# Performance work log

Measured on AMD Instinct MI355X. Metric: run time of the kernel, lower is better.

The kernel has to match this reference:

```python
import jax, jax.numpy as jnp
import numpy as np

N_HEAD = 4
N_FEAT = 256
D_K = N_FEAT // N_HEAD


def setup_inputs() -> dict:
    key = jax.random.key(0)
    ks = jax.random.split(key, 7)
    B, T, F = 8, 2048, N_FEAT
    return {
        "query": jax.random.normal(ks[0], (B, T, F), dtype=jnp.float32),
        "key": jax.random.normal(ks[1], (B, T, F), dtype=jnp.float32),
        "value": jax.random.normal(ks[2], (B, T, F), dtype=jnp.float32),
        "mask": jax.random.randint(ks[3], (B, 1, T), 0, 2, dtype=jnp.int32),
        "W_qkv": jax.random.normal(ks[4], (3 * F, 3 * F), dtype=jnp.float32) * 0.02,
        "b_qkv": jnp.zeros((3 * F,), dtype=jnp.float32),
        "W_out": jax.random.normal(ks[5], (F, F), dtype=jnp.float32) * 0.02,
        "b_out": jnp.zeros((F,), dtype=jnp.float32),
    }


def reference(query, key, value, mask, W_qkv, b_qkv, W_out, b_out):
    B, T, F = query.shape
    H, dk = N_HEAD, D_K
    # fused QKV projection on concatenated [q; k; v]  -> (B, T, 3F)
    qkv = jnp.concatenate([query, key, value], axis=-1) @ W_qkv.T + b_qkv
    qkv = qkv.reshape(B, T, H, 3 * dk)
    q, k, v = jnp.split(qkv, 3, axis=-1)          # each (B, T, H, dk)
    q = q.transpose(0, 2, 1, 3)                    # (B, H, T, dk)
    k = k.transpose(0, 2, 1, 3)
    v = v.transpose(0, 2, 1, 3)
    scores = jnp.einsum("bhqd,bhkd->bhqk", q, k) / jnp.sqrt(jnp.float32(dk))
    # mask: (B, 1, T) -> broadcast (B, 1, 1, T); positions where mask==0 are masked
    m = (mask[:, None, :, :] == 0)
    min_val = jnp.finfo(scores.dtype).min
    scores = jnp.where(m, min_val, scores)
    attn = jax.nn.softmax(scores, axis=-1)
    attn = jnp.where(m, jnp.float32(0.0), attn)    # zero masked probs, as in torch code
    x = jnp.einsum("bhqk,bhkd->bhqd", attn, v)     # (B, H, T, dk)
    x = x.transpose(0, 2, 1, 3).reshape(B, T, H * dk)
    return x @ W_out.T + b_out
```

## Files before the change

### kernel.cpp

```cpp
#include <hip/hip_runtime.h>
#include <hip/hip_bf16.h>

#define NB 8
#define NT 2048
#define NH 4
#define NF 256
#define NTF 768
#define NM (NB * NT)

typedef unsigned short u16;
typedef unsigned int u32;
typedef unsigned long long u64;
typedef u16 u16x8 __attribute__((ext_vector_type(8)));
typedef __bf16 bf16x8 __attribute__((ext_vector_type(8)));
typedef float f32x4 __attribute__((ext_vector_type(4)));
typedef float f32x16 __attribute__((ext_vector_type(16)));

__device__ __forceinline__ u16 bf16_rne(float f) {
    union { float f; unsigned u; } x; x.f = f;
    unsigned u = x.u;
    return (u16)((u + 0x7fffu + ((u >> 16) & 1u)) >> 16);
}

__device__ __forceinline__ int swz(int row, int colB) {
    return row * 128 + (colB ^ ((row & 7) << 4));
}

__device__ __forceinline__ void glds16(const void* g, void* l) {
    __builtin_amdgcn_global_load_lds(
        (const __attribute__((address_space(1))) void*)g,
        (__attribute__((address_space(3))) void*)l, 16, 0, 0);
}

__device__ __forceinline__ u32 pkbf16(float lo, float hi) {
    union { __bf16 h2[2]; u32 u; } t;
    t.h2[0] = (__bf16)lo; t.h2[1] = (__bf16)hi;
    return t.u;
}

__device__ __forceinline__ void pl32swap(u32& a, u32& b) {
    asm("v_permlane32_swap_b32 %0, %1" : "+v"(a), "+v"(b));
}

#define mfma16(A, B, C) __builtin_amdgcn_mfma_f32_16x16x32_bf16((A), (B), (C), 0, 0, 0)
#define mfma32(A, B, C) __builtin_amdgcn_mfma_f32_32x32x16_bf16((A), (B), (C), 0, 0, 0)

__global__ __launch_bounds__(256) void convert_all_kernel(
        const float* __restrict__ q, const float* __restrict__ k,
        const float* __restrict__ v, const float* __restrict__ wqkv,
        const float* __restrict__ wout, const int* __restrict__ mask,
        u16* __restrict__ xcat, u16* __restrict__ wqkvb,
        u16* __restrict__ woutb, float* __restrict__ maskadd) {
    int bid = blockIdx.x;
    if (bid < 6144) {
        int tid = bid * 256 + threadIdx.x;
        int row = tid / 96;
        int c8  = (tid % 96) * 8;
        const float* src; int c;
        if (c8 < NF)            { src = q; c = c8; }
        else if (c8 < 2 * NF)   { src = k; c = c8 - NF; }
        else                    { src = v; c = c8 - 2 * NF; }
        const float4* p = reinterpret_cast<const float4*>(src + (size_t)row * NF + c);
        float4 a = p[0], b = p[1];
        u16x8 o;
        o[0] = bf16_rne(a.x); o[1] = bf16_rne(a.y); o[2] = bf16_rne(a.z); o[3] = bf16_rne(a.w);
        o[4] = bf16_rne(b.x); o[5] = bf16_rne(b.y); o[6] = bf16_rne(b.z); o[7] = bf16_rne(b.w);
        *reinterpret_cast<u16x8*>(xcat + (size_t)row * NTF + c8) = o;
    } else if (bid < 6464) {
        int tid = (bid - 6144) * 256 + threadIdx.x;
        int i8 = tid * 8;
        const float* src; u16* dst; int off;
        if (i8 < NTF * NTF) { src = wqkv; dst = wqkvb; off = i8; }
        else                { src = wout; dst = woutb; off = i8 - NTF * NTF; }
        const float4* p = reinterpret_cast<const float4*>(src + off);
        float4 a = p[0], b = p[1];
        u16x8 o;
        o[0] = bf16_rne(a.x); o[1] = bf16_rne(a.y); o[2] = bf16_rne(a.z); o[3] = bf16_rne(a.w);
        o[4] = bf16_rne(b.x); o[5] = bf16_rne(b.y); o[6] = bf16_rne(b.z); o[7] = bf16_rne(b.w);
        *reinterpret_cast<u16x8*>(dst + off) = o;
    } else {
        int i = (bid - 6464) * 2048 + threadIdx.x * 8;
        int4 m0 = *reinterpret_cast<const int4*>(mask + i);
        int4 m1 = *reinterpret_cast<const int4*>(mask + i + 4);
        float4 f0 = { m0.x ? 0.f : -1e30f, m0.y ? 0.f : -1e30f,
                      m0.z ? 0.f : -1e30f, m0.w ? 0.f : -1e30f };
        float4 f1 = { m1.x ? 0.f : -1e30f, m1.y ? 0.f : -1e30f,
                      m1.z ? 0.f : -1e30f, m1.w ? 0.f : -1e30f };
        *reinterpret_cast<float4*>(maskadd + i) = f0;
        *reinterpret_cast<float4*>(maskadd + i + 4) = f1;
    }
}

template<int N, int K, int MODE>
__global__ __launch_bounds__(256) void gemm128_kernel(
        const u16* __restrict__ A, const u16* __restrict__ Bw,
        const float* __restrict__ bias, void* __restrict__ Cout,
        u16* __restrict__ Vt) {
    __shared__ alignas(16) char smem[65536];
    char* As = smem;
    char* Bs = smem + 32768;
    int m0 = blockIdx.x * 128, n0 = blockIdx.y * 128;
    int tid = threadIdx.x;
    int w = tid >> 6, lane = tid & 63, l15 = lane & 15, hi = lane >> 4;
    int wr = w >> 1, wc = w & 1;
    int r0 = tid >> 3, cb0 = (tid & 7) * 16;
    int gcb = cb0 ^ ((r0 & 7) << 4);
    int wo = w * 1024;

    const char* Ac = (const char*)A;
    const char* Bc = (const char*)Bw;
    const char* gA = Ac + (size_t)(m0 + r0) * (K * 2) + gcb;
    const char* gB = Bc + (size_t)(n0 + r0) * (K * 2) + gcb;
    const size_t rstep = (size_t)32 * (K * 2);

#pragma unroll
    for (int p = 0; p < 4; ++p) {
        glds16(gA + p * rstep, As + p * 4096 + wo);
        glds16(gB + p * rstep, Bs + p * 4096 + wo);
    }

    f32x4 acc[4][4];
#pragma unroll
    for (int fi = 0; fi < 4; ++fi)
#pragma unroll
        for (int fj = 0; fj < 4; ++fj) acc[fi][fj] = (f32x4){0.f, 0.f, 0.f, 0.f};

    constexpr int NKT = K / 64;
    for (int kt = 0; kt < NKT; ++kt) {
        int cur = kt & 1;
        __syncthreads();
        if (kt + 1 < NKT) {
            int off = (kt + 1) * 128;
            char* Ad = As + (cur ^ 1) * 16384;
            char* Bd = Bs + (cur ^ 1) * 16384;
#pragma unroll
            for (int p = 0; p < 4; ++p) {
                glds16(gA + p * rstep + off, Ad + p * 4096 + wo);
                glds16(gB + p * rstep + off, Bd + p * 4096 + wo);
            }
        }
        const char* Ax = As + cur * 16384;
        const char* Bx = Bs + cur * 16384;
#pragma unroll
        for (int ks = 0; ks < 2; ++ks) {
            bf16x8 af[4], bf[4];
#pragma unroll
            for (int fi = 0; fi < 4; ++fi)
                af[fi] = *reinterpret_cast<const bf16x8*>(
                    Ax + swz(wr * 64 + fi * 16 + l15, hi * 16 + ks * 64));
#pragma unroll
            for (int fj = 0; fj < 4; ++fj)
                bf[fj] = *reinterpret_cast<const bf16x8*>(
                    Bx + swz(wc * 64 + fj * 16 + l15, hi * 16 + ks * 64));
#pragma unroll
            for (int fi = 0; fi < 4; ++fi)
#pragma unroll
                for (int fj = 0; fj < 4; ++fj)
                    acc[fi][fj] = mfma16(af[fi], bf[fj], acc[fi][fj]);
        }
    }

    int rowBase = m0 + wr * 64;
    if constexpr (MODE == 2) {
        int g64 = (n0 >> 6) + wc;
        int typ = g64 % 3, h = g64 / 3;
        if (typ == 2) {
            int b = rowBase >> 11;
            int bh = b * NH + h;
#pragma unroll
            for (int fi = 0; fi < 4; ++fi) {
                int t = (rowBase + fi * 16 + hi * 4) & (NT - 1);
#pragma unroll
                for (int fj = 0; fj < 4; ++fj) {
                    int d = fj * 16 + l15;
                    float bv = bias[n0 + wc * 64 + d];
                    u32 lo = pkbf16(acc[fi][fj][0] + bv, acc[fi][fj][1] + bv);
                    u32 hi2 = pkbf16(acc[fi][fj][2] + bv, acc[fi][fj][3] + bv);
                    u64 pk = (u64)lo | ((u64)hi2 << 32);
                    *reinterpret_cast<u64*>(Vt + (size_t)(bh * 64 + d) * NT + t) = pk;
                }
            }
        } else {
#pragma unroll
            for (int fi = 0; fi < 4; ++fi) {
                int orow = rowBase + fi * 16 + hi * 4;
#pragma unroll
                for (int fj = 0; fj < 4; ++fj) {
                    int col = n0 + wc * 64 + fj * 16 + l15;
                    float bv = bias[col];
#pragma unroll
                    for (int r = 0; r < 4; ++r)
                        reinterpret_cast<u16*>(Cout)[(size_t)(orow + r) * N + col] =
                            bf16_rne(acc[fi][fj][r] + bv);
                }
            }
        }
    } else {
#pragma unroll
        for (int fi = 0; fi < 4; ++fi) {
            int orow = rowBase + fi * 16 + hi * 4;
#pragma unroll
            for (int fj = 0; fj < 4; ++fj) {
                int col = n0 + wc * 64 + fj * 16 + l15;
                float bv = bias[col];
#pragma unroll
                for (int r = 0; r < 4; ++r)
                    reinterpret_cast<float*>(Cout)[(size_t)(orow + r) * N + col] =
                        acc[fi][fj][r] + bv;
            }
        }
    }
}

__global__ __launch_bounds__(256, 4) void attn_kernel(
        const u16* __restrict__ qkv, const u16* __restrict__ vt,
        const float* __restrict__ maskadd, u16* __restrict__ xout) {
    int bh = blockIdx.x;
    int q0 = blockIdx.y * 64;
    int b = bh >> 2, h = bh & 3;
    __shared__ alignas(16) char smem[32768];
    int tid = threadIdx.x;
    int w = tid >> 6, lane = tid & 63;
    int l31 = lane & 31, hv = lane >> 5;
    int wq = w & 1, g = w >> 1;
    int r0 = tid >> 3, cb0 = (tid & 7) * 16;
    int gcb = cb0 ^ ((r0 & 7) << 4);
    int wo = w * 1024;
    const float SCALE = 0.125f * 1.44269504088896340736f;

    const char* qkvC = (const char*)qkv;
    const char* vtC  = (const char*)vt;
    const char* gk0 = qkvC + (size_t)(b * NT + r0) * 1536 + h * 384 + 128 + gcb;
    const char* gv0 = vtC + (size_t)(bh * 64 + r0) * (NT * 2) + gcb;
    const float* gm = maskadd + (size_t)b * NT;

    glds16(gk0,              smem + wo);
    glds16(gk0 + 32 * 1536,  smem + 4096 + wo);
    glds16(gv0,              smem + 16384 + wo);
    glds16(gv0 + 32 * 4096,  smem + 16384 + 4096 + wo);

    const char* qrow = qkvC + (size_t)(b * NT + q0 + wq * 32 + l31) * 1536
                       + h * 384 + hv * 16;
    bf16x8 bQ0 = *reinterpret_cast<const bf16x8*>(qrow);
    bf16x8 bQ1 = *reinterpret_cast<const bf16x8*>(qrow + 32);
    bf16x8 bQ2 = *reinterpret_cast<const bf16x8*>(qrow + 64);
    bf16x8 bQ3 = *reinterpret_cast<const bf16x8*>(qrow + 96);

    f32x16 accO0 = 0.f, accO1 = 0.f;
    float ssum = 0.f;

    for (int j = 0; j < NT / 64; ++j) {
        int cur = j & 1;
        __syncthreads();
        if (j < NT / 64 - 1) {
            char* Kd = smem + (cur ^ 1) * 8192;
            char* Vd = smem + 16384 + (cur ^ 1) * 8192;
            size_t ko = (size_t)(j + 1) * 98304;
            size_t vo2 = (size_t)(j + 1) * 128;
            glds16(gk0 + ko,              Kd + wo);
            glds16(gk0 + ko + 32 * 1536,  Kd + 4096 + wo);
            glds16(gv0 + vo2,             Vd + wo);
            glds16(gv0 + vo2 + 32 * 4096, Vd + 4096 + wo);
        }
        const char* Kx = smem + cur * 8192;
        const char* Vx = smem + 16384 + cur * 8192;
        const float* mt = gm + j * 64;

        f32x16 s = 0.f;
        __builtin_amdgcn_s_setprio(1);
#pragma unroll
        for (int ks = 0; ks < 4; ++ks) {
            bf16x8 a = *reinterpret_cast<const bf16x8*>(
                Kx + swz(g * 32 + l31, ks * 32 + hv * 16));
            bf16x8 bq = (ks == 0) ? bQ0 : (ks == 1) ? bQ1 : (ks == 2) ? bQ2 : bQ3;
            s = mfma32(a, bq, s);
        }
        __builtin_amdgcn_s_setprio(0);

#pragma unroll
        for (int rq = 0; rq < 4; ++rq) {
            f32x4 md = *reinterpret_cast<const f32x4*>(mt + g * 32 + rq * 8 + 4 * hv);
#pragma unroll
            for (int e = 0; e < 4; ++e)
                s[rq * 4 + e] = __builtin_amdgcn_exp2f(
                    __builtin_fmaf(s[rq * 4 + e], SCALE, md[e]));
        }
        {
            union { f32x16 v; f32x4 q[4]; } u; u.v = s;
            f32x4 r4 = (u.q[0] + u.q[1]) + (u.q[2] + u.q[3]);
            ssum += (r4[0] + r4[1]) + (r4[2] + r4[3]);
        }
        u32 pa[4], pb[4];
#pragma unroll
        for (int rq = 0; rq < 4; ++rq) {
            pa[rq] = pkbf16(s[rq * 4 + 0], s[rq * 4 + 1]);
            pb[rq] = pkbf16(s[rq * 4 + 2], s[rq * 4 + 3]);
        }
        __builtin_amdgcn_s_setprio(1);
#pragma unroll
        for (int sp2 = 0; sp2 < 2; ++sp2) {
            const int sp = sp2 * 2;
            u32 B0 = pa[sp], B2 = pa[sp + 1], B1 = pb[sp], B3 = pb[sp + 1];
            pl32swap(B0, B2);
            pl32swap(B1, B3);
            union { u32 u4[4]; bf16x8 v; } bp;
            bp.u4[0] = B0; bp.u4[1] = B1; bp.u4[2] = B2; bp.u4[3] = B3;
            int s4 = 2 * g + sp2;
            bf16x8 av0 = *reinterpret_cast<const bf16x8*>(
                Vx + swz(l31, s4 * 32 + hv * 16));
            bf16x8 av1 = *reinterpret_cast<const bf16x8*>(
                Vx + swz(32 + l31, s4 * 32 + hv * 16));
            accO0 = mfma32(av0, bp.v, accO0);
            accO1 = mfma32(av1, bp.v, accO1);
        }
        __builtin_amdgcn_s_setprio(0);
    }

    ssum += __shfl_xor(ssum, 32, 64);
    __syncthreads();
    float* sS = reinterpret_cast<float*>(smem + 16384);
    if (g == 1) {
        union { f32x16 v; f32x4 q[4]; } o0, o1; o0.v = accO0; o1.v = accO1;
#pragma unroll
        for (int i = 0; i < 4; ++i) {
            *reinterpret_cast<f32x4*>(smem + wq * 8192 + i * 1024 + lane * 16) = o0.q[i];
            *reinterpret_cast<f32x4*>(smem + wq * 8192 + (4 + i) * 1024 + lane * 16) = o1.q[i];
        }
        if (lane < 32) sS[wq * 32 + l31] = ssum;
    }
    __syncthreads();
    if (g == 0) {
        union { f32x16 v; f32x4 q[4]; } o0, o1; o0.v = accO0; o1.v = accO1;
#pragma unroll
        for (int i = 0; i < 4; ++i) {
            o0.q[i] += *reinterpret_cast<const f32x4*>(smem + wq * 8192 + i * 1024 + lane * 16);
            o1.q[i] += *reinterpret_cast<const f32x4*>(smem + wq * 8192 + (4 + i) * 1024 + lane * 16);
        }
        float stot = ssum + sS[wq * 32 + l31];
        float inv = stot > 0.f ? 1.0f / stot : 0.0f;
        int qg = b * NT + q0 + wq * 32 + l31;
        const float* of0 = (const float*)&o0.v;
        const float* of1 = (const float*)&o1.v;
#pragma unroll
        for (int db = 0; db < 2; ++db) {
            const float* of = db ? of1 : of0;
#pragma unroll
            for (int rq = 0; rq < 4; ++rq) {
                u32 lo = pkbf16(of[rq * 4 + 0] * inv, of[rq * 4 + 1] * inv);
                u32 hi2 = pkbf16(of[rq * 4 + 2] * inv, of[rq * 4 + 3] * inv);
                u64 pk = (u64)lo | ((u64)hi2 << 32);
                int d = db * 32 + rq * 8 + 4 * hv;
                *reinterpret_cast<u64*>(xout + (size_t)qg * NF + h * 64 + d) = pk;
            }
        }
    }
}

extern "C" void kernel_launch(void* const* d_in, const int* in_sizes, int n_in,
                              void* d_out, int out_size, void* d_ws, size_t ws_size,
                              hipStream_t stream) {
    const float* q    = (const float*)d_in[0];
    const float* k    = (const float*)d_in[1];
    const float* v    = (const float*)d_in[2];
    const int*   mask = (const int*)d_in[3];
    const float* wqkv = (const float*)d_in[4];
    const float* bqkv = (const float*)d_in[5];
    const float* wout = (const float*)d_in[6];
    const float* bout = (const float*)d_in[7];
    float* out = (float*)d_out;

    char* ws = (char*)d_ws;
    u16*   Xcat    = (u16*)(ws);
    u16*   QKV     = (u16*)(ws + 25165824);
    u16*   Vt      = (u16*)(ws + 50331648);
    u16*   Xattn   = (u16*)(ws + 58720256);
    u16*   Wqkvb   = (u16*)(ws + 67108864);
    u16*   Woutb   = (u16*)(ws + 68288512);
    float* Maskadd = (float*)(ws + 68419584);

    convert_all_kernel<<<6472, 256, 0, stream>>>(q, k, v, wqkv, wout, mask,
                                                 Xcat, Wqkvb, Woutb, Maskadd);
    gemm128_kernel<NTF, NTF, 2><<<dim3(NM / 128, NTF / 128), 256, 0, stream>>>(
        Xcat, Wqkvb, bqkv, QKV, Vt);
    attn_kernel<<<dim3(NB * NH, NT / 64), 256, 0, stream>>>(QKV, Vt, Maskadd, Xattn);
    gemm128_kernel<NF, NF, 1><<<dim3(NM / 128, NF / 128), 256, 0, stream>>>(
        Xattn, Woutb, bout, out, nullptr);
}
```

Measured before the change: 105.1 us.

## Triple-buffer K/V tiles with explicit vmcnt waits and prefetch mask values

The attention loop's K/V shared-memory staging goes from double to triple buffering, so each tile is fetched two iterations ahead. The full __syncthreads is replaced by hand-placed s_waitcnt vmcnt counts plus a raw s_barrier. Mask values for the next tile are also loaded into registers one iteration ahead, instead of read from global memory inside the softmax step. The aim is to hide global-load latency better, at the cost of raising LDS to 48KB and lowering the launch-bounds occupancy hint from 4 to 3 blocks per CU. The manual vmcnt accounting is fragile if the compiler reorders or adds memory ops.

```diff
diff --git a/kernel.cpp b/kernel.cpp
--- a/kernel.cpp
+++ b/kernel.cpp
@@ -212,13 +212,13 @@
     }
 }
 
-__global__ __launch_bounds__(256, 4) void attn_kernel(
+__global__ __launch_bounds__(256, 3) void attn_kernel(
         const u16* __restrict__ qkv, const u16* __restrict__ vt,
         const float* __restrict__ maskadd, u16* __restrict__ xout) {
     int bh = blockIdx.x;
     int q0 = blockIdx.y * 64;
     int b = bh >> 2, h = bh & 3;
-    __shared__ alignas(16) char smem[32768];
+    __shared__ alignas(16) char smem[49152];
     int tid = threadIdx.x;
     int w = tid >> 6, lane = tid & 63;
     int l31 = lane & 31, hv = lane >> 5;
@@ -234,10 +234,15 @@
     const char* gv0 = vtC + (size_t)(bh * 64 + r0) * (NT * 2) + gcb;
     const float* gm = maskadd + (size_t)b * NT;
 
-    glds16(gk0,              smem + wo);
-    glds16(gk0 + 32 * 1536,  smem + 4096 + wo);
-    glds16(gv0,              smem + 16384 + wo);
-    glds16(gv0 + 32 * 4096,  smem + 16384 + 4096 + wo);
+    auto stage = [&](int t) {
+        char* Kd = smem + (t % 3) * 8192;
+        char* Vd = smem + 24576 + (t % 3) * 8192;
+        size_t ko = (size_t)t * 98304, vo2 = (size_t)t * 128;
+        glds16(gk0 + ko,                      Kd + wo);
+        glds16(gk0 + ko + (size_t)32 * 1536,  Kd + 4096 + wo);
+        glds16(gv0 + vo2,                     Vd + wo);
+        glds16(gv0 + vo2 + (size_t)32 * 4096, Vd + 4096 + wo);
+    };
 
     const char* qrow = qkvC + (size_t)(b * NT + q0 + wq * 32 + l31) * 1536
                        + h * 384 + hv * 16;
@@ -246,25 +251,34 @@
     bf16x8 bQ2 = *reinterpret_cast<const bf16x8*>(qrow + 64);
     bf16x8 bQ3 = *reinterpret_cast<const bf16x8*>(qrow + 96);
 
+    f32x4 mcur[4], mnext[4];
+#pragma unroll
+    for (int rq = 0; rq < 4; ++rq)
+        mcur[rq] = *reinterpret_cast<const f32x4*>(gm + g * 32 + rq * 8 + 4 * hv);
+    stage(0);
+    stage(1);
+
     f32x16 accO0 = 0.f, accO1 = 0.f;
     float ssum = 0.f;
 
     for (int j = 0; j < NT / 64; ++j) {
-        int cur = j & 1;
-        __syncthreads();
+        if (j == 0 || j == NT / 64 - 1)
+            asm volatile("s_waitcnt vmcnt(4)" ::: "memory");
+        else
+            asm volatile("s_waitcnt vmcnt(8)" ::: "memory");
+        __builtin_amdgcn_s_barrier();
+        __builtin_amdgcn_sched_barrier(0);
+
         if (j < NT / 64 - 1) {
-            char* Kd = smem + (cur ^ 1) * 8192;
-            char* Vd = smem + 16384 + (cur ^ 1) * 8192;
-            size_t ko = (size_t)(j + 1) * 98304;
-            size_t vo2 = (size_t)(j + 1) * 128;
-            glds16(gk0 + ko,              Kd + wo);
-            glds16(gk0 + ko + 32 * 1536,  Kd + 4096 + wo);
-            glds16(gv0 + vo2,             Vd + wo);
-            glds16(gv0 + vo2 + 32 * 4096, Vd + 4096 + wo);
-        }
-        const char* Kx = smem + cur * 8192;
-        const char* Vx = smem + 16384 + cur * 8192;
-        const float* mt = gm + j * 64;
+#pragma unroll
+            for (int rq = 0; rq < 4; ++rq)
+                mnext[rq] = *reinterpret_cast<const f32x4*>(
+                    gm + (j + 1) * 64 + g * 32 + rq * 8 + 4 * hv);
+        }
+        if (j < NT / 64 - 2) stage(j + 2);
+
+        const char* Kx = smem + (j % 3) * 8192;
+        const char* Vx = smem + 24576 + (j % 3) * 8192;
 
         f32x16 s = 0.f;
         __builtin_amdgcn_s_setprio(1);
@@ -279,11 +293,10 @@
 
 #pragma unroll
         for (int rq = 0; rq < 4; ++rq) {
-            f32x4 md = *reinterpret_cast<const f32x4*>(mt + g * 32 + rq * 8 + 4 * hv);
 #pragma unroll
             for (int e = 0; e < 4; ++e)
                 s[rq * 4 + e] = __builtin_amdgcn_exp2f(
-                    __builtin_fmaf(s[rq * 4 + e], SCALE, md[e]));
+                    __builtin_fmaf(s[rq * 4 + e], SCALE, mcur[rq][e]));
         }
         {
             union { f32x16 v; f32x4 q[4]; } u; u.v = s;
@@ -314,6 +327,8 @@
             accO1 = mfma32(av1, bp.v, accO1);
         }
         __builtin_amdgcn_s_setprio(0);
+#pragma unroll
+        for (int rq = 0; rq < 4; ++rq) mcur[rq] = mnext[rq];
     }
 
     ssum += __shfl_xor(ssum, 32, 64);
```

After: 111.4 us. +6.0%, slower.

## Process 128 queries per attention block to reuse K/V tiles twice

Applied to the files above, without the earlier changes.

Each attention workgroup now handles 128 query rows instead of 64: every wave keeps two sets of Q fragments and accumulators, so each K and V tile loaded into shared memory feeds twice as many MFMAs. This halves global K/V traffic and per-tile load and sync overhead. In exchange the grid shrinks to 512 blocks, register pressure rises (launch bounds lowered from 4 to 3 blocks per SM), and the reduction scratch in shared memory grows slightly.

```diff
diff --git a/kernel.cpp b/kernel.cpp
--- a/kernel.cpp
+++ b/kernel.cpp
@@ -212,13 +212,13 @@
     }
 }
 
-__global__ __launch_bounds__(256, 4) void attn_kernel(
+__global__ __launch_bounds__(256, 3) void attn_kernel(
         const u16* __restrict__ qkv, const u16* __restrict__ vt,
         const float* __restrict__ maskadd, u16* __restrict__ xout) {
     int bh = blockIdx.x;
-    int q0 = blockIdx.y * 64;
+    int q0 = blockIdx.y * 128;
     int b = bh >> 2, h = bh & 3;
-    __shared__ alignas(16) char smem[32768];
+    __shared__ alignas(16) char smem[33280];
     int tid = threadIdx.x;
     int w = tid >> 6, lane = tid & 63;
     int l31 = lane & 31, hv = lane >> 5;
@@ -239,15 +239,20 @@
     glds16(gv0,              smem + 16384 + wo);
     glds16(gv0 + 32 * 4096,  smem + 16384 + 4096 + wo);
 
-    const char* qrow = qkvC + (size_t)(b * NT + q0 + wq * 32 + l31) * 1536
-                       + h * 384 + hv * 16;
-    bf16x8 bQ0 = *reinterpret_cast<const bf16x8*>(qrow);
-    bf16x8 bQ1 = *reinterpret_cast<const bf16x8*>(qrow + 32);
-    bf16x8 bQ2 = *reinterpret_cast<const bf16x8*>(qrow + 64);
-    bf16x8 bQ3 = *reinterpret_cast<const bf16x8*>(qrow + 96);
-
-    f32x16 accO0 = 0.f, accO1 = 0.f;
-    float ssum = 0.f;
+    const char* qrow0 = qkvC + (size_t)(b * NT + q0 + wq * 64 + l31) * 1536
+                        + h * 384 + hv * 16;
+    const char* qrow1 = qrow0 + (size_t)32 * 1536;
+    bf16x8 bQ00 = *reinterpret_cast<const bf16x8*>(qrow0);
+    bf16x8 bQ01 = *reinterpret_cast<const bf16x8*>(qrow0 + 32);
+    bf16x8 bQ02 = *reinterpret_cast<const bf16x8*>(qrow0 + 64);
+    bf16x8 bQ03 = *reinterpret_cast<const bf16x8*>(qrow0 + 96);
+    bf16x8 bQ10 = *reinterpret_cast<const bf16x8*>(qrow1);
+    bf16x8 bQ11 = *reinterpret_cast<const bf16x8*>(qrow1 + 32);
+    bf16x8 bQ12 = *reinterpret_cast<const bf16x8*>(qrow1 + 64);
+    bf16x8 bQ13 = *reinterpret_cast<const bf16x8*>(qrow1 + 96);
+
+    f32x16 acc00 = 0.f, acc01 = 0.f, acc10 = 0.f, acc11 = 0.f;
+    float ssum0 = 0.f, ssum1 = 0.f;
 
     for (int j = 0; j < NT / 64; ++j) {
         int cur = j & 1;
@@ -266,14 +271,16 @@
         const char* Vx = smem + 16384 + cur * 8192;
         const float* mt = gm + j * 64;
 
-        f32x16 s = 0.f;
+        f32x16 s0 = 0.f, s1 = 0.f;
         __builtin_amdgcn_s_setprio(1);
 #pragma unroll
         for (int ks = 0; ks < 4; ++ks) {
             bf16x8 a = *reinterpret_cast<const bf16x8*>(
                 Kx + swz(g * 32 + l31, ks * 32 + hv * 16));
-            bf16x8 bq = (ks == 0) ? bQ0 : (ks == 1) ? bQ1 : (ks == 2) ? bQ2 : bQ3;
-            s = mfma32(a, bq, s);
+            bf16x8 bq0 = (ks == 0) ? bQ00 : (ks == 1) ? bQ01 : (ks == 2) ? bQ02 : bQ03;
+            bf16x8 bq1 = (ks == 0) ? bQ10 : (ks == 1) ? bQ11 : (ks == 2) ? bQ12 : bQ13;
+            s0 = mfma32(a, bq0, s0);
+            s1 = mfma32(a, bq1, s1);
         }
         __builtin_amdgcn_s_setprio(0);
 
@@ -281,77 +288,111 @@
         for (int rq = 0; rq < 4; ++rq) {
             f32x4 md = *reinterpret_cast<const f32x4*>(mt + g * 32 + rq * 8 + 4 * hv);
 #pragma unroll
-            for (int e = 0; e < 4; ++e)
-                s[rq * 4 + e] = __builtin_amdgcn_exp2f(
-                    __builtin_fmaf(s[rq * 4 + e], SCALE, md[e]));
+            for (int e = 0; e < 4; ++e) {
+                s0[rq * 4 + e] = __builtin_amdgcn_exp2f(
+                    __builtin_fmaf(s0[rq * 4 + e], SCALE, md[e]));
+                s1[rq * 4 + e] = __builtin_amdgcn_exp2f(
+                    __builtin_fmaf(s1[rq * 4 + e], SCALE, md[e]));
+            }
         }
         {
-            union { f32x16 v; f32x4 q[4]; } u; u.v = s;
-            f32x4 r4 = (u.q[0] + u.q[1]) + (u.q[2] + u.q[3]);
-            ssum += (r4[0] + r4[1]) + (r4[2] + r4[3]);
-        }
-        u32 pa[4], pb[4];
+            union { f32x16 v; f32x4 q[4]; } u0, u1; u0.v = s0; u1.v = s1;
+            f32x4 r0v = (u0.q[0] + u0.q[1]) + (u0.q[2] + u0.q[3]);
+            f32x4 r1v = (u1.q[0] + u1.q[1]) + (u1.q[2] + u1.q[3]);
+            ssum0 += (r0v[0] + r0v[1]) + (r0v[2] + r0v[3]);
+            ssum1 += (r1v[0] + r1v[1]) + (r1v[2] + r1v[3]);
+        }
+        u32 pa0[4], pb0[4], pa1[4], pb1[4];
 #pragma unroll
         for (int rq = 0; rq < 4; ++rq) {
-            pa[rq] = pkbf16(s[rq * 4 + 0], s[rq * 4 + 1]);
-            pb[rq] = pkbf16(s[rq * 4 + 2], s[rq * 4 + 3]);
+            pa0[rq] = pkbf16(s0[rq * 4 + 0], s0[rq * 4 + 1]);
+            pb0[rq] = pkbf16(s0[rq * 4 + 2], s0[rq * 4 + 3]);
+            pa1[rq] = pkbf16(s1[rq * 4 + 0], s1[rq * 4 + 1]);
+            pb1[rq] = pkbf16(s1[rq * 4 + 2], s1[rq * 4 + 3]);
         }
         __builtin_amdgcn_s_setprio(1);
 #pragma unroll
         for (int sp2 = 0; sp2 < 2; ++sp2) {
             const int sp = sp2 * 2;
-            u32 B0 = pa[sp], B2 = pa[sp + 1], B1 = pb[sp], B3 = pb[sp + 1];
-            pl32swap(B0, B2);
-            pl32swap(B1, B3);
-            union { u32 u4[4]; bf16x8 v; } bp;
-            bp.u4[0] = B0; bp.u4[1] = B1; bp.u4[2] = B2; bp.u4[3] = B3;
             int s4 = 2 * g + sp2;
             bf16x8 av0 = *reinterpret_cast<const bf16x8*>(
                 Vx + swz(l31, s4 * 32 + hv * 16));
             bf16x8 av1 = *reinterpret_cast<const bf16x8*>(
                 Vx + swz(32 + l31, s4 * 32 + hv * 16));
-            accO0 = mfma32(av0, bp.v, accO0);
-            accO1 = mfma32(av1, bp.v, accO1);
+            u32 A0 = pa0[sp], A2 = pa0[sp + 1], A1 = pb0[sp], A3 = pb0[sp + 1];
+            pl32swap(A0, A2);
+            pl32swap(A1, A3);
+            union { u32 u4[4]; bf16x8 v; } bp0;
+            bp0.u4[0] = A0; bp0.u4[1] = A1; bp0.u4[2] = A2; bp0.u4[3] = A3;
+            u32 C0 = pa1[sp], C2 = pa1[sp + 1], C1 = pb1[sp], C3 = pb1[sp + 1];
+            pl32swap(C0, C2);
+            pl32swap(C1, C3);
+            union { u32 u4[4]; bf16x8 v; } bp1;
+            bp1.u4[0] = C0; bp1.u4[1] = C1; bp1.u4[2] = C2; bp1.u4[3] = C3;
+            acc00 = mfma32(av0, bp0.v, acc00);
+            acc01 = mfma32(av1, bp0.v, acc01);
+            acc10 = mfma32(av0, bp1.v, acc10);
+            acc11 = mfma32(av1, bp1.v, acc11);
         }
         __builtin_amdgcn_s_setprio(0);
     }
 
-    ssum += __shfl_xor(ssum, 32, 64);
+    ssum0 += __shfl_xor(ssum0, 32, 64);
+    ssum1 += __shfl_xor(ssum1, 32, 64);
     __syncthreads();
-    float* sS = reinterpret_cast<float*>(smem + 16384);
+    float* sS = reinterpret_cast<float*>(smem + 32768);
     if (g == 1) {
-        union { f32x16 v; f32x4 q[4]; } o0, o1; o0.v = accO0; o1.v = accO1;
+        union { f32x16 v; f32x4 q[4]; } a00, a01, a10, a11;
+        a00.v = acc00; a01.v = acc01; a10.v = acc10; a11.v = acc11;
 #pragma unroll
         for (int i = 0; i < 4; ++i) {
-            *reinterpret_cast<f32x4*>(smem + wq * 8192 + i * 1024 + lane * 16) = o0.q[i];
-            *reinterpret_cast<f32x4*>(smem + wq * 8192 + (4 + i) * 1024 + lane * 16) = o1.q[i];
-        }
-        if (lane < 32) sS[wq * 32 + l31] = ssum;
+            *reinterpret_cast<f32x4*>(smem + (wq * 2 + 0) * 8192 + i * 1024 + lane * 16) = a00.q[i];
+            *reinterpret_cast<f32x4*>(smem + (wq * 2 + 0) * 8192 + (4 + i) * 1024 + lane * 16) = a01.q[i];
+            *reinterpret_cast<f32x4*>(smem + (wq * 2 + 1) * 8192 + i * 1024 + lane * 16) = a10.q[i];
+            *reinterpret_cast<f32x4*>(smem + (wq * 2 + 1) * 8192 + (4 + i) * 1024 + lane * 16) = a11.q[i];
+        }
+        if (lane < 32) {
+            sS[(wq * 2 + 0) * 32 + l31] = ssum0;
+            sS[(wq * 2 + 1) * 32 + l31] = ssum1;
+        }
     }
     __syncthreads();
     if (g == 0) {
-        union { f32x16 v; f32x4 q[4]; } o0, o1; o0.v = accO0; o1.v = accO1;
+        union { f32x16 v; f32x4 q[4]; } a00, a01, a10, a11;
+        a00.v = acc00; a01.v = acc01; a10.v = acc10; a11.v = acc11;
 #pragma unroll
         for (int i = 0; i < 4; ++i) {
-            o0.q[i] += *reinterpret_cast<const f32x4*>(smem + wq * 8192 + i * 1024 + lane * 16);
-            o1.q[i] += *reinterpret_cast<const f32x4*>(smem + wq * 8192 + (4 + i) * 1024 + lane * 16);
-        }
-        float stot = ssum + sS[wq * 32 + l31];
-        float inv = stot > 0.f ? 1.0f / stot : 0.0f;
-        int qg = b * NT + q0 + wq * 32 + l31;
-        const float* of0 = (const float*)&o0.v;
-        const float* of1 = (const float*)&o1.v;
-#pragma unroll
-        for (int db = 0; db < 2; ++db) {
-            const float* of = db ? of1 : of0;
-#pragma unroll
-            for (int rq = 0; rq < 4; ++rq) {
-                u32 lo = pkbf16(of[rq * 4 + 0] * inv, of[rq * 4 + 1] * inv);
-                u32 hi2 = pkbf16(of[rq * 4 + 2] * inv, of[rq * 4 + 3] * inv);
-                u64 pk = (u64)lo | ((u64)hi2 << 32);
-                int d = db * 32 + rq * 8 + 4 * hv;
-                *reinterpret_cast<u64*>(xout + (size_t)qg * NF + h * 64 + d) = pk;
-            }
+            a00.q[i] += *reinterpret_cast<const f32x4*>(smem + (wq * 2 + 0) * 8192 + i * 1024 + lane * 16);
+            a01.q[i] += *reinterpret_cast<const f32x4*>(smem + (wq * 2 + 0) * 8192 + (4 + i) * 1024 + lane * 16);
+            a10.q[i] += *reinterpret_cast<const f32x4*>(smem + (wq * 2 + 1) * 8192 + i * 1024 + lane * 16);
+            a11.q[i] += *reinterpret_cast<const f32x4*>(smem + (wq * 2 + 1) * 8192 + (4 + i) * 1024 + lane * 16);
+        }
+        float st0 = ssum0 + sS[(wq * 2 + 0) * 32 + l31];
+        float st1 = ssum1 + sS[(wq * 2 + 1) * 32 + l31];
+        float inv0 = st0 > 0.f ? 1.0f / st0 : 0.0f;
+        float inv1 = st1 > 0.f ? 1.0f / st1 : 0.0f;
+        int qg0 = b * NT + q0 + wq * 64 + l31;
+        int qg1 = qg0 + 32;
+        const float* f00 = (const float*)&a00.v;
+        const float* f01 = (const float*)&a01.v;
+        const float* f10 = (const float*)&a10.v;
+        const float* f11 = (const float*)&a11.v;
+#pragma unroll
+        for (int rq = 0; rq < 4; ++rq) {
+            int d0 = rq * 8 + 4 * hv;
+            u64 pk;
+            pk = (u64)pkbf16(f00[rq * 4 + 0] * inv0, f00[rq * 4 + 1] * inv0)
+               | ((u64)pkbf16(f00[rq * 4 + 2] * inv0, f00[rq * 4 + 3] * inv0) << 32);
+            *reinterpret_cast<u64*>(xout + (size_t)qg0 * NF + h * 64 + d0) = pk;
+            pk = (u64)pkbf16(f01[rq * 4 + 0] * inv0, f01[rq * 4 + 1] * inv0)
+               | ((u64)pkbf16(f01[rq * 4 + 2] * inv0, f01[rq * 4 + 3] * inv0) << 32);
+            *reinterpret_cast<u64*>(xout + (size_t)qg0 * NF + h * 64 + 32 + d0) = pk;
+            pk = (u64)pkbf16(f10[rq * 4 + 0] * inv1, f10[rq * 4 + 1] * inv1)
+               | ((u64)pkbf16(f10[rq * 4 + 2] * inv1, f10[rq * 4 + 3] * inv1) << 32);
+            *reinterpret_cast<u64*>(xout + (size_t)qg1 * NF + h * 64 + d0) = pk;
+            pk = (u64)pkbf16(f11[rq * 4 + 0] * inv1, f11[rq * 4 + 1] * inv1)
+               | ((u64)pkbf16(f11[rq * 4 + 2] * inv1, f11[rq * 4 + 3] * inv1) << 32);
+            *reinterpret_cast<u64*>(xout + (size_t)qg1 * NF + h * 64 + 32 + d0) = pk;
         }
     }
 }
@@ -382,7 +423,7 @@
                                                  Xcat, Wqkvb, Woutb, Maskadd);
     gemm128_kernel<NTF, NTF, 2><<<dim3(NM / 128, NTF / 128), 256, 0, stream>>>(
         Xcat, Wqkvb, bqkv, QKV, Vt);
-    attn_kernel<<<dim3(NB * NH, NT / 64), 256, 0, stream>>>(QKV, Vt, Maskadd, Xattn);
+    attn_kernel<<<dim3(NB * NH, NT / 128), 256, 0, stream>>>(QKV, Vt, Maskadd, Xattn);
     gemm128_kernel<NF, NF, 1><<<dim3(NM / 128, NF / 128), 256, 0, stream>>>(
         Xattn, Woutb, bout, out, nullptr);
 }
```

After: 107.1 us. No clear change (+1.9%).
